# Performance work log

Measured on AMD Instinct MI355X. Metric: run time of the kernel, lower is better.

Reference implementation:

```python
import jax, jax.numpy as jnp
import numpy as np

B, S, DIM = 4, 1024, 2048
HQ, HKV, HD = 16, 4, 128  # query heads, kv heads, head dim
G = HQ // HKV             # GQA group size


def _rope(t, freqs):
    # t: (B, S, H, HD); freqs: (S, HD//2) angles. Llama-style: adjacent pairs
    # (even, odd) treated as (real, imag) and rotated by exp(i*theta).
    tr = t.reshape(t.shape[:-1] + (HD // 2, 2))
    cos = jnp.cos(freqs)[None, :, None, :]
    sin = jnp.sin(freqs)[None, :, None, :]
    re = tr[..., 0] * cos - tr[..., 1] * sin
    im = tr[..., 0] * sin + tr[..., 1] * cos
    return jnp.stack([re, im], axis=-1).reshape(t.shape)


def setup_inputs() -> dict:
    key = jax.random.key(0)
    ks = jax.random.split(key, 5)
    x = jax.random.normal(ks[0], (B, S, DIM), jnp.float32)
    # rotary angles: outer(t, 1/10000^(2i/d))
    inv_freq = 1.0 / (10000.0 ** (np.arange(0, HD, 2, dtype=np.float32) / HD))
    freqs = jnp.asarray(np.outer(np.arange(S, dtype=np.float32), inv_freq))
    # additive causal mask (finite large negative for numerical safety)
    i = jnp.arange(S)
    mask = jnp.where(i[None, :] <= i[:, None], 0.0, -1e9).astype(jnp.float32)
    std = 0.02
    wq = jax.random.normal(ks[1], (HQ * HD, DIM), jnp.float32) * std
    wk = jax.random.normal(ks[2], (HKV * HD, DIM), jnp.float32) * std
    wv = jax.random.normal(ks[3], (HKV * HD, DIM), jnp.float32) * std
    wo = jax.random.normal(ks[4], (DIM, DIM), jnp.float32) * std
    return {"x": x, "start_pos": 0, "freqs": freqs, "mask": mask,
            "wq": wq, "wk": wk, "wv": wv, "wo": wo}


def reference(x, start_pos, freqs, mask, wq, wk, wv, wo):
    b, s, _ = x.shape
    q = (x @ wq.T).reshape(b, s, HQ, HD)
    k = (x @ wk.T).reshape(b, s, HKV, HD)
    v = (x @ wv.T).reshape(b, s, HKV, HD)
    q = _rope(q, freqs)
    k = _rope(k, freqs)
    # GQA: group query heads per kv head, avoiding repeat_kv materialization
    qg = q.reshape(b, s, HKV, G, HD)
    scores = jnp.einsum('bskgd,btkd->bkgst', qg, k) / np.float32(np.sqrt(HD))
    scores = scores + mask  # (S,S) broadcasts over (b, kv, g, s, t)
    p = jax.nn.softmax(scores, axis=-1)
    o = jnp.einsum('bkgst,btkd->bskgd', p, v).reshape(b, s, HQ * HD)
    return o @ wo.T
```

## Files before the change

### kernel.cpp

```cpp
#include <hip/hip_runtime.h>

typedef unsigned short u16;
typedef unsigned int u32;
typedef __bf16 bf16x8 __attribute__((ext_vector_type(8)));
typedef float floatx4 __attribute__((ext_vector_type(4)));

#if __has_builtin(__builtin_amdgcn_exp2f)
#define EXP2F(x) __builtin_amdgcn_exp2f(x)
#else
#define EXP2F(x) __expf((x) * 0.6931471805599453f)
#endif

__device__ __forceinline__ u16 f2bf(float x) {
  union { float f; u32 u; } v; v.f = x;
  u32 r = v.u + 0x7fffu + ((v.u >> 16) & 1u);
  return (u16)(r >> 16);
}
__device__ __forceinline__ float bf2f(u16 x) {
  union { float f; u32 u; } v; v.u = ((u32)x) << 16;
  return v.f;
}

__device__ __forceinline__ void gl_lds16(const u16* g, u16* l) {
  __builtin_amdgcn_global_load_lds((const __attribute__((address_space(1))) void*)g,
                                   (__attribute__((address_space(3))) void*)l, 16, 0, 0);
}

__global__ __launch_bounds__(256) void cvt_all(const float* __restrict__ x,
                                               const float* __restrict__ wq,
                                               const float* __restrict__ wk,
                                               const float* __restrict__ wv,
                                               const float* __restrict__ wo,
                                               u16* __restrict__ xb, u16* __restrict__ wqb,
                                               u16* __restrict__ wkb, u16* __restrict__ wvb,
                                               u16* __restrict__ wob) {
  int i = blockIdx.x * 256 + threadIdx.x;
  const float* s; u16* d; int off;
  if (i < 2097152)      { s = x;  d = xb;  off = 0; }
  else if (i < 3145728) { s = wq; d = wqb; off = 2097152; }
  else if (i < 3407872) { s = wk; d = wkb; off = 3145728; }
  else if (i < 3670016) { s = wv; d = wvb; off = 3407872; }
  else                  { s = wo; d = wob; off = 3670016; }
  i -= off;
  float4 v = ((const float4*)s)[i];
  uint2 o;
  o.x = (u32)f2bf(v.x) | ((u32)f2bf(v.y) << 16);
  o.y = (u32)f2bf(v.z) | ((u32)f2bf(v.w) << 16);
  ((uint2*)d)[i] = o;
}

__global__ __launch_bounds__(256) void rope_both(u16* __restrict__ qb, u16* __restrict__ kb,
                                                 const float* __restrict__ fr) {
  int idx = blockIdx.x * 256 + threadIdx.x;
  u16* t; int lgH; float scale;
  if (idx < 4194304) { t = qb; lgH = 4; scale = 0.08838834764831845f * 1.4426950408889634f; }
  else               { t = kb; lgH = 2; scale = 1.0f; idx -= 4194304; }
  int p = idx & 63;
  int bsh = idx >> 6;
  int s = (bsh >> lgH) & 1023;
  float th = fr[s * 64 + p];
  float sn, cs;
  sincosf(th, &sn, &cs);
  u32* base = (u32*)(t + (size_t)bsh * 128 + p * 2);
  u32 pr = *base;
  float e = bf2f((u16)(pr & 0xffffu));
  float o = bf2f((u16)(pr >> 16));
  u16 re = f2bf((e * cs - o * sn) * scale);
  u16 im = f2bf((e * sn + o * cs) * scale);
  *base = (u32)re | ((u32)im << 16);
}

__device__ __forceinline__ void gemm_core(const u16* __restrict__ A, const u16* __restrict__ Bw,
                                          u16* sA, u16* sB, int m0, int n0,
                                          floatx4 acc[4][4]) {
  const int tid = threadIdx.x;
  const int wave = tid >> 6, lane = tid & 63;
  const int quad = lane >> 4, l16 = lane & 15;
  const int wm = (wave >> 1) * 64, wn = (wave & 1) * 64;
  const int srow = wave * 8 + (lane >> 3);
  const int scol = (((lane & 7) ^ ((lane >> 3) & 7)) * 8);
  const int lds_off = wave * 512 + lane * 8;
  const int swA = (l16 & 7);
  for (int k0 = 0; k0 < 2048; k0 += 64) {
    __syncthreads();
    #pragma unroll
    for (int c = 0; c < 4; c++) {
      gl_lds16(A + (size_t)(m0 + c * 32 + srow) * 2048 + k0 + scol, sA + c * 2048 + lds_off);
      gl_lds16(Bw + (size_t)(n0 + c * 32 + srow) * 2048 + k0 + scol, sB + c * 2048 + lds_off);
    }
    __syncthreads();
    #pragma unroll
    for (int ks = 0; ks < 64; ks += 32) {
      const int pc = ((((ks >> 3) + quad) ^ swA) << 3);
      bf16x8 af[4], bw[4];
      #pragma unroll
      for (int i = 0; i < 4; i++)
        af[i] = *(const bf16x8*)&sA[(wm + i * 16 + l16) * 64 + pc];
      #pragma unroll
      for (int j = 0; j < 4; j++)
        bw[j] = *(const bf16x8*)&sB[(wn + j * 16 + l16) * 64 + pc];
      #pragma unroll
      for (int i = 0; i < 4; i++)
        #pragma unroll
        for (int j = 0; j < 4; j++)
          acc[i][j] = __builtin_amdgcn_mfma_f32_16x16x32_bf16(af[i], bw[j], acc[i][j], 0, 0, 0);
    }
  }
}

__global__ __launch_bounds__(256, 3) void gemm_qkv(const u16* __restrict__ xb,
                                                   const u16* __restrict__ wqb,
                                                   const u16* __restrict__ wkb,
                                                   const u16* __restrict__ wvb,
                                                   u16* __restrict__ qb, u16* __restrict__ kb,
                                                   u16* __restrict__ vtb) {
  __shared__ __align__(16) u16 sA[128 * 64];
  __shared__ __align__(16) u16 sB[128 * 64];
  const int by = blockIdx.y;
  const u16* Bw; int n0, mode;
  if (by < 16)      { Bw = wqb; n0 = by * 128;        mode = 0; }
  else if (by < 20) { Bw = wkb; n0 = (by - 16) * 128; mode = 1; }
  else              { Bw = wvb; n0 = (by - 20) * 128; mode = 2; }
  const int m0 = blockIdx.x * 128;
  floatx4 acc[4][4] = {};
  gemm_core(xb, Bw, sA, sB, m0, n0, acc);
  const int tid = threadIdx.x;
  const int wave = tid >> 6, lane = tid & 63;
  const int quad = lane >> 4, l16 = lane & 15;
  const int wm = (wave >> 1) * 64, wn = (wave & 1) * 64;
  #pragma unroll
  for (int i = 0; i < 4; i++) {
    #pragma unroll
    for (int j = 0; j < 4; j++) {
      const int row0 = m0 + wm + i * 16 + quad * 4;
      const int col = n0 + wn + j * 16 + l16;
      #pragma unroll
      for (int r = 0; r < 4; r++) {
        int m = row0 + r;
        u16 val = f2bf(acc[i][j][r]);
        if (mode == 0) {
          qb[(size_t)m * 2048 + col] = val;
        } else if (mode == 1) {
          kb[(size_t)m * 512 + col] = val;
        } else {
          int b = m >> 10, sI = m & 1023, kvh = col >> 7, hd = col & 127;
          vtb[((size_t)((b * 4 + kvh) * 128 + hd)) * 1024 + sI] = val;
        }
      }
    }
  }
}

__global__ __launch_bounds__(256, 3) void gemm_out(const u16* __restrict__ ob,
                                                   const u16* __restrict__ wob,
                                                   float* __restrict__ Cf) {
  __shared__ __align__(16) u16 sA[128 * 64];
  __shared__ __align__(16) u16 sB[128 * 64];
  const int m0 = blockIdx.x * 128, n0 = blockIdx.y * 128;
  floatx4 acc[4][4] = {};
  gemm_core(ob, wob, sA, sB, m0, n0, acc);
  const int tid = threadIdx.x;
  const int wave = tid >> 6, lane = tid & 63;
  const int quad = lane >> 4, l16 = lane & 15;
  const int wm = (wave >> 1) * 64, wn = (wave & 1) * 64;
  #pragma unroll
  for (int i = 0; i < 4; i++) {
    #pragma unroll
    for (int j = 0; j < 4; j++) {
      const int row0 = m0 + wm + i * 16 + quad * 4;
      const int col = n0 + wn + j * 16 + l16;
      #pragma unroll
      for (int r = 0; r < 4; r++)
        Cf[(size_t)(row0 + r) * 2048 + col] = acc[i][j][r];
    }
  }
}

__device__ __forceinline__ void store_out(u16* __restrict__ obaseHead, int qr0,
                                          floatx4 (&o_acc)[2][8], float (&l_part)[2],
                                          int quad, int l16) {
  #pragma unroll
  for (int i = 0; i < 2; i++) {
    float lr = l_part[i];
    lr += __shfl_xor(lr, 16);
    lr += __shfl_xor(lr, 32);
    #pragma unroll
    for (int r = 0; r < 4; r++) {
      const float inv = 1.f / __shfl(lr, quad * 4 + r);
      const int row = qr0 + i * 16 + quad * 4 + r;
      #pragma unroll
      for (int j = 0; j < 8; j++)
        obaseHead[(size_t)row * 2048 + j * 16 + l16] = f2bf(o_acc[i][j][r] * inv);
    }
  }
}

__global__ __launch_bounds__(256)
__attribute__((amdgpu_waves_per_eu(2, 2)))
void flash_attn(const u16* __restrict__ q,
                const u16* __restrict__ k,
                const u16* __restrict__ vt,
                u16* __restrict__ o) {
  __shared__ __align__(16) u16 sK[2][64 * 128];
  __shared__ __align__(16) u16 sV[128 * 64];
  __shared__ __align__(16) u16 sP[4][32 * 64];
  const int tid = threadIdx.x;
  const int wave = tid >> 6, lane = tid & 63;
  const int quad = lane >> 4, l16 = lane & 15;
  const int bi = blockIdx.x;
  const int bkv = bi & 15;
  const int b = bkv >> 2, kv = bkv & 3;
  const int hp = (bi >> 4) & 1;
  const int u = bi >> 5;
  const int m = (u < 8) ? u : 23 - u;
  const int qh = kv * 4 + hp * 2 + (wave >> 1);
  const int qr0 = m * 64 + (wave & 1) * 32;

  const u16* qbase = q + (size_t)b * 2097152 + qh * 128;
  const u16* vbase = vt + (size_t)(b * 4 + kv) * 131072;
  u16* obase = o + (size_t)b * 2097152 + qh * 128;
  u16* myP = &sP[wave][0];

  bf16x8 aq[2][4];
  #pragma unroll
  for (int i = 0; i < 2; i++)
    #pragma unroll
    for (int ks = 0; ks < 4; ks++)
      aq[i][ks] = *(const bf16x8*)(qbase + (size_t)(qr0 + i * 16 + l16) * 2048 + ks * 32 + quad * 8);

  floatx4 o_acc[2][8];
  float l_part[2];
  const floatx4 vzero = {0.f, 0.f, 0.f, 0.f};
  #pragma unroll
  for (int i = 0; i < 2; i++) {
    l_part[i] = 0.f;
    #pragma unroll
    for (int j = 0; j < 8; j++) o_acc[i][j] = vzero;
  }

  #define STAGE_K(T, PAR)                                                         \
    {                                                                             \
      const u16* kb_t = k + (size_t)(b * 1024 + (T) * 64) * 512 + kv * 128;       \
      _Pragma("unroll")                                                           \
      for (int v = 0; v < 4; v++) {                                               \
        int ci = v * 256 + tid;                                                   \
        int r = ci >> 4, c = ci & 15;                                             \
        gl_lds16(kb_t + r * 512 + ((c ^ (r & 7)) << 3), &sK[PAR][ci * 8]);        \
      }                                                                           \
    }
  #define STAGE_V(T)                                                              \
    {                                                                             \
      _Pragma("unroll")                                                           \
      for (int v = 0; v < 4; v++) {                                               \
        int ci = v * 256 + tid;                                                   \
        int r = ci >> 3, c = ci & 7;                                              \
        gl_lds16(vbase + r * 1024 + (T) * 64 + ((c ^ (r & 7)) << 3), &sV[ci * 8]); \
      }                                                                           \
    }

  STAGE_K(0, 0);
  __syncthreads();

  for (int t = 0; t <= m; t++) {
    STAGE_V(t);
    if (t < m) STAGE_K(t + 1, (t + 1) & 1);

    const u16* kcur = &sK[t & 1][0];
    floatx4 s_acc[4][2];
    #pragma unroll
    for (int j = 0; j < 4; j++)
      #pragma unroll
      for (int i = 0; i < 2; i++) s_acc[j][i] = vzero;
    bf16x8 bkA[4], bkB[4];
    #pragma unroll
    for (int j = 0; j < 4; j++) {
      const int R = j * 16 + l16;
      bkA[j] = *(const bf16x8*)&kcur[R * 128 + ((quad ^ (R & 7)) << 3)];
    }
    #pragma unroll
    for (int ks = 0; ks < 4; ks++) {
      bf16x8* cur = (ks & 1) ? bkB : bkA;
      bf16x8* nxt = (ks & 1) ? bkA : bkB;
      if (ks < 3) {
        #pragma unroll
        for (int j = 0; j < 4; j++) {
          const int R = j * 16 + l16;
          nxt[j] = *(const bf16x8*)&kcur[R * 128 + ((((ks + 1) * 4 + quad) ^ (R & 7)) << 3)];
        }
      }
      #pragma unroll
      for (int j = 0; j < 4; j++)
        #pragma unroll
        for (int i = 0; i < 2; i++)
          s_acc[j][i] = __builtin_amdgcn_mfma_f32_16x16x32_bf16(cur[j], aq[i][ks], s_acc[j][i], 0, 0, 0);
    }

    const bool nomask = (t < m);
    #pragma unroll
    for (int i = 0; i < 2; i++) {
      const int qrow = qr0 + i * 16 + l16;
      #pragma unroll
      for (int j = 0; j < 4; j++) {
        const int key0 = t * 64 + j * 16 + quad * 4;
        float e0, e1, e2, e3;
        if (nomask) {
          e0 = EXP2F(s_acc[j][i][0]);
          e1 = EXP2F(s_acc[j][i][1]);
          e2 = EXP2F(s_acc[j][i][2]);
          e3 = EXP2F(s_acc[j][i][3]);
        } else {
          e0 = (key0 + 0 <= qrow) ? EXP2F(s_acc[j][i][0]) : 0.f;
          e1 = (key0 + 1 <= qrow) ? EXP2F(s_acc[j][i][1]) : 0.f;
          e2 = (key0 + 2 <= qrow) ? EXP2F(s_acc[j][i][2]) : 0.f;
          e3 = (key0 + 3 <= qrow) ? EXP2F(s_acc[j][i][3]) : 0.f;
        }
        l_part[i] += (e0 + e1) + (e2 + e3);
        uint2 w;
        w.x = (u32)f2bf(e0) | ((u32)f2bf(e1) << 16);
        w.y = (u32)f2bf(e2) | ((u32)f2bf(e3) << 16);
        const int ri = i * 16 + l16;
        *(uint2*)&myP[ri * 64 + (((2 * j + (quad >> 1)) ^ (ri & 7)) << 3) + (quad & 1) * 4] = w;
      }
    }

    __syncthreads();

    #pragma unroll
    for (int ks2 = 0; ks2 < 2; ks2++) {
      bf16x8 ap[2], bvf[8];
      #pragma unroll
      for (int j2 = 0; j2 < 8; j2++) {
        const int R = j2 * 16 + l16;
        bvf[j2] = *(const bf16x8*)&sV[R * 64 + (((ks2 * 4 + quad) ^ (R & 7)) << 3)];
      }
      #pragma unroll
      for (int i = 0; i < 2; i++) {
        const int ri = i * 16 + l16;
        ap[i] = *(const bf16x8*)&myP[ri * 64 + (((ks2 * 4 + quad) ^ (ri & 7)) << 3)];
      }
      #pragma unroll
      for (int i = 0; i < 2; i++)
        #pragma unroll
        for (int j2 = 0; j2 < 8; j2++)
          o_acc[i][j2] = __builtin_amdgcn_mfma_f32_16x16x32_bf16(ap[i], bvf[j2], o_acc[i][j2], 0, 0, 0);
    }

    __syncthreads();
  }

  store_out(obase, qr0, o_acc, l_part, quad, l16);
  #undef STAGE_K
  #undef STAGE_V
}

extern "C" void kernel_launch(void* const* d_in, const int* in_sizes, int n_in,
                              void* d_out, int out_size, void* d_ws, size_t ws_size,
                              hipStream_t stream) {
  const float* x  = (const float*)d_in[0];
  const float* fr = (const float*)d_in[2];
  const float* wq = (const float*)d_in[4];
  const float* wk = (const float*)d_in[5];
  const float* wv = (const float*)d_in[6];
  const float* wo = (const float*)d_in[7];
  float* out = (float*)d_out;

  char* ws = (char*)d_ws;
  u16* xb  = (u16*)(ws + 0);
  u16* wqb = (u16*)(ws + 16777216);
  u16* wkb = (u16*)(ws + 25165824);
  u16* wvb = (u16*)(ws + 27262976);
  u16* wob = (u16*)(ws + 29360128);
  u16* qb  = (u16*)(ws + 37748736);
  u16* kb  = (u16*)(ws + 54525952);
  u16* vtb = (u16*)(ws + 58720256);
  u16* ob  = (u16*)(ws + 62914560);

  cvt_all<<<18432, 256, 0, stream>>>(x, wq, wk, wv, wo, xb, wqb, wkb, wvb, wob);
  gemm_qkv<<<dim3(32, 24), 256, 0, stream>>>(xb, wqb, wkb, wvb, qb, kb, vtb);
  rope_both<<<20480, 256, 0, stream>>>(qb, kb, fr);
  flash_attn<<<512, 256, 0, stream>>>(qb, kb, vtb, ob);
  gemm_out<<<dim3(32, 16), 256, 0, stream>>>(ob, wob, out);
}
```

Before: 267.0 us.

## Rewrite projection GEMMs as 8-wave 128x256 tiles with triple-buffered LDS pipeline

Replaces the 4-wave 128x128 GEMM core with an 8-wave 128x256 tile. Global-to-LDS loads are triple-buffered, with two K-tiles prefetched ahead and explicit vmcnt waits. Those loads are interleaved with LDS reads and MFMA phases separated by barriers, and s_setprio raises priority during MFMA phases. The goal is to hide global load latency, which the old core exposed with two __syncthreads per K-step and no prefetch, and to improve B-operand reuse. In exchange it uses far more LDS (144KB per block), allows fewer blocks per CU and launches half as many blocks, which may cause occupancy and tail-wave imbalance.

```diff
diff --git a/kernel.cpp b/kernel.cpp
--- a/kernel.cpp
+++ b/kernel.cpp
@@ -10,6 +10,8 @@
 #else
 #define EXP2F(x) __expf((x) * 0.6931471805599453f)
 #endif
+
+#define MFMA16(d, a, b) d = __builtin_amdgcn_mfma_f32_16x16x32_bf16(a, b, d, 0, 0, 0)
 
 __device__ __forceinline__ u16 f2bf(float x) {
   union { float f; u32 u; } v; v.f = x;
@@ -70,64 +72,123 @@
   *base = (u32)re | ((u32)im << 16);
 }
 
-__device__ __forceinline__ void gemm_core(const u16* __restrict__ A, const u16* __restrict__ Bw,
-                                          u16* sA, u16* sB, int m0, int n0,
-                                          floatx4 acc[4][4]) {
+__device__ __forceinline__ void gemm8_core(const u16* __restrict__ A,
+                                           const u16* __restrict__ Bw,
+                                           int m0, int n0,
+                                           u16* sA, u16* sB,
+                                           floatx4 (&acc)[4][4]) {
   const int tid = threadIdx.x;
   const int wave = tid >> 6, lane = tid & 63;
   const int quad = lane >> 4, l16 = lane & 15;
-  const int wm = (wave >> 1) * 64, wn = (wave & 1) * 64;
-  const int srow = wave * 8 + (lane >> 3);
-  const int scol = (((lane & 7) ^ ((lane >> 3) & 7)) * 8);
-  const int lds_off = wave * 512 + lane * 8;
-  const int swA = (l16 & 7);
-  for (int k0 = 0; k0 < 2048; k0 += 64) {
-    __syncthreads();
-    #pragma unroll
-    for (int c = 0; c < 4; c++) {
-      gl_lds16(A + (size_t)(m0 + c * 32 + srow) * 2048 + k0 + scol, sA + c * 2048 + lds_off);
-      gl_lds16(Bw + (size_t)(n0 + c * 32 + srow) * 2048 + k0 + scol, sB + c * 2048 + lds_off);
-    }
-    __syncthreads();
-    #pragma unroll
-    for (int ks = 0; ks < 64; ks += 32) {
-      const int pc = ((((ks >> 3) + quad) ^ swA) << 3);
-      bf16x8 af[4], bw[4];
-      #pragma unroll
-      for (int i = 0; i < 4; i++)
-        af[i] = *(const bf16x8*)&sA[(wm + i * 16 + l16) * 64 + pc];
-      #pragma unroll
-      for (int j = 0; j < 4; j++)
-        bw[j] = *(const bf16x8*)&sB[(wn + j * 16 + l16) * 64 + pc];
-      #pragma unroll
-      for (int i = 0; i < 4; i++)
-        #pragma unroll
-        for (int j = 0; j < 4; j++)
-          acc[i][j] = __builtin_amdgcn_mfma_f32_16x16x32_bf16(af[i], bw[j], acc[i][j], 0, 0, 0);
-    }
-  }
-}
-
-__global__ __launch_bounds__(256, 3) void gemm_qkv(const u16* __restrict__ xb,
-                                                   const u16* __restrict__ wqb,
-                                                   const u16* __restrict__ wkb,
-                                                   const u16* __restrict__ wvb,
-                                                   u16* __restrict__ qb, u16* __restrict__ kb,
-                                                   u16* __restrict__ vtb) {
-  __shared__ __align__(16) u16 sA[128 * 64];
-  __shared__ __align__(16) u16 sB[128 * 64];
+  const int wm = (wave >> 2) * 64, wn = (wave & 3) * 64;
+  const int swk = l16 & 7;
+
+#define G8_STAGE_A(T)                                                          \
+  {                                                                            \
+    u16* dst = sA + ((T) % 3) * 8192;                                          \
+    const u16* src = A + (size_t)m0 * 2048 + (T) * 64;                         \
+    _Pragma("unroll")                                                          \
+    for (int v = 0; v < 2; v++) {                                              \
+      int ci = v * 512 + tid;                                                  \
+      int r = ci >> 3, c = ci & 7;                                             \
+      gl_lds16(src + (size_t)r * 2048 + ((c ^ (r & 7)) << 3), dst + ci * 8);   \
+    }                                                                          \
+  }
+#define G8_STAGE_B(T, H)                                                       \
+  {                                                                            \
+    u16* dst = sB + ((T) % 3) * 16384;                                         \
+    const u16* src = Bw + (size_t)n0 * 2048 + (T) * 64;                        \
+    _Pragma("unroll")                                                          \
+    for (int v = 2 * (H); v < 2 * (H) + 2; v++) {                              \
+      int ci = v * 512 + tid;                                                  \
+      int r = ci >> 3, c = ci & 7;                                             \
+      gl_lds16(src + (size_t)r * 2048 + ((c ^ (r & 7)) << 3), dst + ci * 8);   \
+    }                                                                          \
+  }
+
+  G8_STAGE_A(0); G8_STAGE_B(0, 0); G8_STAGE_B(0, 1);
+  G8_STAGE_A(1); G8_STAGE_B(1, 0); G8_STAGE_B(1, 1);
+
+  for (int t = 0; t < 32; t++) {
+    const u16* cA = sA + (t % 3) * 8192;
+    const u16* cB = sB + (t % 3) * 16384;
+    if (t < 31) { asm volatile("s_waitcnt vmcnt(6)" ::: "memory"); }
+    else        { asm volatile("s_waitcnt vmcnt(0)" ::: "memory"); }
+    __builtin_amdgcn_sched_barrier(0);
+    __builtin_amdgcn_s_barrier();
+    bf16x8 af[4], bw[2];
+    #pragma unroll
+    for (int i = 0; i < 4; i++)
+      af[i] = *(const bf16x8*)&cA[(wm + i * 16 + l16) * 64 + ((quad ^ swk) << 3)];
+    #pragma unroll
+    for (int j = 0; j < 2; j++)
+      bw[j] = *(const bf16x8*)&cB[(wn + j * 16 + l16) * 64 + ((quad ^ swk) << 3)];
+    if (t + 2 < 32) G8_STAGE_A(t + 2);
+    __builtin_amdgcn_s_barrier();
+    __builtin_amdgcn_s_setprio(1);
+    #pragma unroll
+    for (int i = 0; i < 4; i++) { MFMA16(acc[i][0], af[i], bw[0]); MFMA16(acc[i][1], af[i], bw[1]); }
+    __builtin_amdgcn_s_setprio(0);
+    __builtin_amdgcn_s_barrier();
+    #pragma unroll
+    for (int j = 0; j < 2; j++)
+      bw[j] = *(const bf16x8*)&cB[(wn + (j + 2) * 16 + l16) * 64 + ((quad ^ swk) << 3)];
+    if (t + 2 < 32) G8_STAGE_B(t + 2, 0);
+    __builtin_amdgcn_s_barrier();
+    __builtin_amdgcn_s_setprio(1);
+    #pragma unroll
+    for (int i = 0; i < 4; i++) { MFMA16(acc[i][2], af[i], bw[0]); MFMA16(acc[i][3], af[i], bw[1]); }
+    __builtin_amdgcn_s_setprio(0);
+    __builtin_amdgcn_s_barrier();
+    #pragma unroll
+    for (int i = 0; i < 4; i++)
+      af[i] = *(const bf16x8*)&cA[(wm + i * 16 + l16) * 64 + (((4 + quad) ^ swk) << 3)];
+    #pragma unroll
+    for (int j = 0; j < 2; j++)
+      bw[j] = *(const bf16x8*)&cB[(wn + j * 16 + l16) * 64 + (((4 + quad) ^ swk) << 3)];
+    if (t + 2 < 32) G8_STAGE_B(t + 2, 1);
+    __builtin_amdgcn_s_barrier();
+    __builtin_amdgcn_s_setprio(1);
+    #pragma unroll
+    for (int i = 0; i < 4; i++) { MFMA16(acc[i][0], af[i], bw[0]); MFMA16(acc[i][1], af[i], bw[1]); }
+    __builtin_amdgcn_s_setprio(0);
+    __builtin_amdgcn_s_barrier();
+    #pragma unroll
+    for (int j = 0; j < 2; j++)
+      bw[j] = *(const bf16x8*)&cB[(wn + (j + 2) * 16 + l16) * 64 + (((4 + quad) ^ swk) << 3)];
+    __builtin_amdgcn_s_barrier();
+    __builtin_amdgcn_s_setprio(1);
+    #pragma unroll
+    for (int i = 0; i < 4; i++) { MFMA16(acc[i][2], af[i], bw[0]); MFMA16(acc[i][3], af[i], bw[1]); }
+    __builtin_amdgcn_s_setprio(0);
+    __builtin_amdgcn_s_barrier();
+  }
+#undef G8_STAGE_A
+#undef G8_STAGE_B
+}
+
+__global__ __launch_bounds__(512)
+__attribute__((amdgpu_waves_per_eu(2, 2)))
+void gemm_qkv(const u16* __restrict__ xb,
+              const u16* __restrict__ wqb,
+              const u16* __restrict__ wkb,
+              const u16* __restrict__ wvb,
+              u16* __restrict__ qb, u16* __restrict__ kb,
+              u16* __restrict__ vtb) {
+  __shared__ __align__(16) u16 sA[3 * 128 * 64];
+  __shared__ __align__(16) u16 sB[3 * 256 * 64];
   const int by = blockIdx.y;
   const u16* Bw; int n0, mode;
-  if (by < 16)      { Bw = wqb; n0 = by * 128;        mode = 0; }
-  else if (by < 20) { Bw = wkb; n0 = (by - 16) * 128; mode = 1; }
-  else              { Bw = wvb; n0 = (by - 20) * 128; mode = 2; }
+  if (by < 8)       { Bw = wqb; n0 = by * 256;        mode = 0; }
+  else if (by < 10) { Bw = wkb; n0 = (by - 8) * 256;  mode = 1; }
+  else              { Bw = wvb; n0 = (by - 10) * 256; mode = 2; }
   const int m0 = blockIdx.x * 128;
   floatx4 acc[4][4] = {};
-  gemm_core(xb, Bw, sA, sB, m0, n0, acc);
+  gemm8_core(xb, Bw, m0, n0, sA, sB, acc);
   const int tid = threadIdx.x;
   const int wave = tid >> 6, lane = tid & 63;
   const int quad = lane >> 4, l16 = lane & 15;
-  const int wm = (wave >> 1) * 64, wn = (wave & 1) * 64;
+  const int wm = (wave >> 2) * 64, wn = (wave & 3) * 64;
   #pragma unroll
   for (int i = 0; i < 4; i++) {
     #pragma unroll
@@ -151,18 +212,20 @@
   }
 }
 
-__global__ __launch_bounds__(256, 3) void gemm_out(const u16* __restrict__ ob,
-                                                   const u16* __restrict__ wob,
-                                                   float* __restrict__ Cf) {
-  __shared__ __align__(16) u16 sA[128 * 64];
-  __shared__ __align__(16) u16 sB[128 * 64];
-  const int m0 = blockIdx.x * 128, n0 = blockIdx.y * 128;
+__global__ __launch_bounds__(512)
+__attribute__((amdgpu_waves_per_eu(2, 2)))
+void gemm_out(const u16* __restrict__ ob,
+              const u16* __restrict__ wob,
+              float* __restrict__ Cf) {
+  __shared__ __align__(16) u16 sA[3 * 128 * 64];
+  __shared__ __align__(16) u16 sB[3 * 256 * 64];
+  const int m0 = blockIdx.x * 128, n0 = blockIdx.y * 256;
   floatx4 acc[4][4] = {};
-  gemm_core(ob, wob, sA, sB, m0, n0, acc);
+  gemm8_core(ob, wob, m0, n0, sA, sB, acc);
   const int tid = threadIdx.x;
   const int wave = tid >> 6, lane = tid & 63;
   const int quad = lane >> 4, l16 = lane & 15;
-  const int wm = (wave >> 1) * 64, wn = (wave & 1) * 64;
+  const int wm = (wave >> 2) * 64, wn = (wave & 3) * 64;
   #pragma unroll
   for (int i = 0; i < 4; i++) {
     #pragma unroll
@@ -376,8 +439,8 @@
   u16* ob  = (u16*)(ws + 62914560);
 
   cvt_all<<<18432, 256, 0, stream>>>(x, wq, wk, wv, wo, xb, wqb, wkb, wvb, wob);
-  gemm_qkv<<<dim3(32, 24), 256, 0, stream>>>(xb, wqb, wkb, wvb, qb, kb, vtb);
+  gemm_qkv<<<dim3(32, 12), 512, 0, stream>>>(xb, wqb, wkb, wvb, qb, kb, vtb);
   rope_both<<<20480, 256, 0, stream>>>(qb, kb, fr);
   flash_attn<<<512, 256, 0, stream>>>(qb, kb, vtb, ob);
-  gemm_out<<<dim3(32, 16), 256, 0, stream>>>(ob, wob, out);
-}
+  gemm_out<<<dim3(32, 8), 512, 0, stream>>>(ob, wob, out);
+}
```

Result: slower. 308.6 us (+15.6%).
